# Kernel optimization log

Measured on AMD Instinct MI355X. Metric: run time of the kernel, lower is better.

Reference implementation:

```python
import jax, jax.numpy as jnp
import numpy as np

B, N, D, H = 256, 128, 2048, 16
DH = D // H  # 128 == N, required by the module's broadcast coefs*out


def setup_inputs() -> dict:
    key = jax.random.key(0)
    k0, k1, k2, k3, k4, k5 = jax.random.split(key, 6)
    batchinput = jax.random.normal(k0, (B, N, D), dtype=jnp.float32)
    # Conv1d(D, DH, 1, bias=False) == pointwise linear D -> DH
    Wa = jax.random.normal(k1, (D, DH), dtype=jnp.float32) * 0.02
    # Conv1d(DH, 1, 1) with bias
    Wb = jax.random.normal(k2, (DH, 1), dtype=jnp.float32) * 0.02
    bb = jax.random.normal(k3, (1,), dtype=jnp.float32) * 0.02
    Wc = jax.random.normal(k4, (DH, 1), dtype=jnp.float32) * 0.02
    bc = jax.random.normal(k5, (1,), dtype=jnp.float32) * 0.02
    bias = jnp.full((DH,), 0.01, dtype=jnp.float32)
    return {"batchinput": batchinput, "Wa": Wa, "Wb": Wb, "bb": bb,
            "Wc": Wc, "bc": bc, "bias": bias}


def reference(batchinput, Wa, Wb, bb, Wc, bc, bias):
    # All n_head heads share weights and dropout=0 -> identical; mean over heads
    # equals a single head. n_steps=1 (multi-step is shape-incompatible for H>1).
    h = jnp.einsum("bnd,de->bne", batchinput, Wa)          # [B,N,DH]
    t1 = h @ Wb + bb                                        # [B,N,1]
    t2 = h @ Wc + bc                                        # [B,N,1]
    # torch: temp1.permute -> [B,N,1]; temp2 stays [B,1,N]; broadcast add
    scores = t1 + jnp.swapaxes(t2, 1, 2)                    # [B,N,N]
    # F.softmax with dim=None on a 3D tensor -> dim=1
    coefs = jax.nn.softmax(jax.nn.leaky_relu(scores, negative_slope=0.2), axis=1)
    re = coefs * h + bias                                   # [B,N,N]*[B,N,DH], DH==N
    re = re + h                                             # residual=True
    return re
```

## Files before the change

### kernel.cpp

```cpp
#include <hip/hip_runtime.h>
#include <hip/hip_bf16.h>
#include <stdint.h>

typedef short bf16x8 __attribute__((ext_vector_type(8)));
typedef float f32x4  __attribute__((ext_vector_type(4)));

__device__ __forceinline__ unsigned short f2bf(float f) {
  unsigned int u = __float_as_uint(f);
  u = (u + 0x7fffu + ((u >> 16) & 1u)) >> 16;
  return (unsigned short)u;
}
__device__ __forceinline__ float bf2f(unsigned short s) { return __uint_as_float(((unsigned int)s) << 16); }
__device__ __forceinline__ float bflo(unsigned int pr) { return __uint_as_float(pr << 16); }
__device__ __forceinline__ float bfhi(unsigned int pr) { return __uint_as_float(pr & 0xffff0000u); }

#define Nn 128
#define Dd 2048
#define DH 128
#define BK 64
#define HP 130

__global__ void detect_dtype(const unsigned int* __restrict__ X, int* __restrict__ flag) {
  if (threadIdx.x == 0) {
    int cnt = 0;
#pragma unroll
    for (int i = 0; i < 64; ++i) {
      unsigned int e = (X[i] >> 23) & 0xffu;
      cnt += (e < 200u) ? 1 : 0;
    }
    *flag = (cnt >= 32) ? 1 : 0;
  }
}

__global__ __launch_bounds__(256) void transpose_wa(const void* __restrict__ Wa,
                                                    short* __restrict__ WaT,
                                                    const int* __restrict__ flag) {
  const int f32 = *flag;
  __shared__ short tile[32][33];
  const int tx = threadIdx.x & 31, ty = threadIdx.x >> 5;
  const int d0 = blockIdx.x * 32, e0 = blockIdx.y * 32;
#pragma unroll
  for (int r = 0; r < 4; ++r) {
    const int src = (d0 + ty + 8 * r) * DH + e0 + tx;
    short v;
    if (f32) v = (short)f2bf(((const float*)Wa)[src]);
    else     v = ((const short*)Wa)[src];
    tile[ty + 8 * r][tx] = v;
  }
  __syncthreads();
#pragma unroll
  for (int r = 0; r < 4; ++r)
    WaT[(e0 + ty + 8 * r) * Dd + d0 + tx] = tile[tx][ty + 8 * r];
}

union SMemU {
  struct { short A[128 * BK]; short Bm[128 * BK]; } st;
  unsigned short h[128 * HP];
};

template <bool F32>
__device__ __forceinline__ void gat_body(
    const void* __restrict__ Xv, const short* __restrict__ WaT,
    const void* __restrict__ Wb, const void* __restrict__ bbp,
    const void* __restrict__ Wc, const void* __restrict__ bcp,
    const void* __restrict__ biasp, void* __restrict__ outv,
    SMemU& sm, float* t1s, float* t2s, float* wbs, float* wcs,
    float* biass, float* red, float* mrec, float* srec)
{
  const int tid = threadIdx.x;
  const int b   = blockIdx.x;
  const int l   = tid & 63;
  const int w   = tid >> 6;
  const int wr  = w >> 1, wcol = w & 1;

  if (tid < 128) {
    wbs[tid]   = F32 ? ((const float*)Wb)[tid]    : bf2f(((const unsigned short*)Wb)[tid]);
    wcs[tid]   = F32 ? ((const float*)Wc)[tid]    : bf2f(((const unsigned short*)Wc)[tid]);
    biass[tid] = F32 ? ((const float*)biasp)[tid] : bf2f(((const unsigned short*)biasp)[tid]);
  }

  f32x4 acc[4][4];
#pragma unroll
  for (int i = 0; i < 4; ++i)
#pragma unroll
    for (int j = 0; j < 4; ++j) acc[i][j] = (f32x4){0.f, 0.f, 0.f, 0.f};

  const int rowi = tid >> 3;
  const int kofs = (tid & 7) * 8;
  short* As = sm.st.A;
  short* Bs = sm.st.Bm;
  const size_t xbase = (size_t)b * Nn * Dd;

  bf16x8 aV[4], bV[4];
  auto load_tiles = [&](int k0) {
#pragma unroll
    for (int c = 0; c < 4; ++c) {
      const int grow = (32 * c + rowi) * Dd + k0 + kofs;
      if (F32) {
        const float* p = (const float*)Xv + xbase + grow;
        float4 u0 = *(const float4*)p;
        float4 u1 = *(const float4*)(p + 4);
        bf16x8 t;
        t[0] = (short)f2bf(u0.x); t[1] = (short)f2bf(u0.y);
        t[2] = (short)f2bf(u0.z); t[3] = (short)f2bf(u0.w);
        t[4] = (short)f2bf(u1.x); t[5] = (short)f2bf(u1.y);
        t[6] = (short)f2bf(u1.z); t[7] = (short)f2bf(u1.w);
        aV[c] = t;
      } else {
        aV[c] = *(const bf16x8*)((const short*)Xv + xbase + grow);
      }
      bV[c] = *(const bf16x8*)(WaT + grow);
    }
  };

  load_tiles(0);
  for (int k0 = 0; k0 < Dd; k0 += BK) {
    __syncthreads();
#pragma unroll
    for (int c = 0; c < 4; ++c) {
      *(bf16x8*)&As[c * 2048 + tid * 8] = aV[c];
      *(bf16x8*)&Bs[c * 2048 + tid * 8] = bV[c];
    }
    __syncthreads();
    if (k0 + BK < Dd) load_tiles(k0 + BK);
#pragma unroll
    for (int ks = 0; ks < 2; ++ks) {
      bf16x8 aF[4], bF[4];
#pragma unroll
      for (int mr = 0; mr < 4; ++mr)
        aF[mr] = *(const bf16x8*)&As[(wr * 64 + mr * 16 + (l & 15)) * BK + ks * 32 + (l >> 4) * 8];
#pragma unroll
      for (int nc = 0; nc < 4; ++nc)
        bF[nc] = *(const bf16x8*)&Bs[(wcol * 64 + nc * 16 + (l & 15)) * BK + ks * 32 + (l >> 4) * 8];
#pragma unroll
      for (int mr = 0; mr < 4; ++mr)
#pragma unroll
        for (int nc = 0; nc < 4; ++nc)
          acc[mr][nc] = __builtin_amdgcn_mfma_f32_16x16x32_bf16(aF[mr], bF[nc], acc[mr][nc], 0, 0, 0);
    }
  }
  __syncthreads();

#pragma unroll
  for (int mr = 0; mr < 4; ++mr) {
    const int row0 = wr * 64 + mr * 16 + (l >> 4) * 4;
#pragma unroll
    for (int nc = 0; nc < 4; ++nc) {
      const int col = wcol * 64 + nc * 16 + (l & 15);
#pragma unroll
      for (int r = 0; r < 4; ++r)
        sm.h[(row0 + r) * HP + col] = f2bf(acc[mr][nc][r]);
    }
  }
  __syncthreads();

  {
    const int i = tid & 127;
    const float* wv = (tid < 128) ? wbs : wcs;
    const unsigned int* hr = (const unsigned int*)&sm.h[i * HP];
    float a0 = 0.f, a1 = 0.f;
#pragma unroll 4
    for (int e2 = 0; e2 < 64; ++e2) {
      const unsigned int pr = hr[e2];
      a0 += bflo(pr) * wv[2 * e2];
      a1 += bfhi(pr) * wv[2 * e2 + 1];
    }
    const void* bsel = (tid < 128) ? bbp : bcp;
    const float bbv = F32 ? ((const float*)bsel)[0] : bf2f(((const unsigned short*)bsel)[0]);
    const float t = a0 + a1 + bbv;
    if (tid < 128) t1s[i] = t; else t2s[i] = t;
  }
  __syncthreads();

  {
    const int j  = tid & 127;
    const int hf = tid >> 7;
    const float t2j = t2s[j];
    float mloc = -1e30f;
#pragma unroll 4
    for (int ii = 0; ii < 64; ++ii) {
      float s = t1s[hf * 64 + ii] + t2j;
      s = (s > 0.f) ? s : 0.2f * s;
      mloc = fmaxf(mloc, s);
    }
    red[hf * 128 + j] = mloc;
    __syncthreads();
    const float mj = fmaxf(red[j], red[128 + j]);
    float sl = 0.f;
#pragma unroll 4
    for (int ii = 0; ii < 64; ++ii) {
      float s = t1s[hf * 64 + ii] + t2j;
      s = (s > 0.f) ? s : 0.2f * s;
      sl += __expf(s - mj);
    }
    __syncthreads();
    red[hf * 128 + j] = sl;
    __syncthreads();
    if (hf == 0) {
      mrec[j] = mj;
      srec[j] = 1.f / (red[j] + red[128 + j]);
    }
  }
  __syncthreads();

  {
    const int jp = (tid & 63) * 2;
    const int rq = tid >> 6;
    const float m0 = mrec[jp],     s0 = srec[jp];
    const float m1 = mrec[jp + 1], s1 = srec[jp + 1];
    const float u0 = t2s[jp], u1 = t2s[jp + 1];
    const float b0 = biass[jp], b1 = biass[jp + 1];
#pragma unroll 4
    for (int ii = 0; ii < 32; ++ii) {
      const int i = ii * 4 + rq;
      const float t1i = t1s[i];
      float sA = t1i + u0; sA = (sA > 0.f) ? sA : 0.2f * sA;
      float sB = t1i + u1; sB = (sB > 0.f) ? sB : 0.2f * sB;
      const float pA = __expf(sA - m0) * s0;
      const float pB = __expf(sB - m1) * s1;
      const unsigned int pr = *(const unsigned int*)&sm.h[i * HP + jp];
      const float oA = bflo(pr) * (1.f + pA) + b0;
      const float oB = bfhi(pr) * (1.f + pB) + b1;
      if (F32) {
        float2 v2; v2.x = oA; v2.y = oB;
        *(float2*)((float*)outv + (size_t)b * Nn * DH + i * DH + jp) = v2;
      } else {
        const unsigned int pk = (unsigned int)f2bf(oA) | ((unsigned int)f2bf(oB) << 16);
        *(unsigned int*)((unsigned short*)outv + (size_t)b * Nn * DH + i * DH + jp) = pk;
      }
    }
  }
}

__global__ __launch_bounds__(256, 1) void fused_gat(
    const void* __restrict__ X, const short* __restrict__ WaT,
    const void* __restrict__ Wb, const void* __restrict__ bb,
    const void* __restrict__ Wc, const void* __restrict__ bc,
    const void* __restrict__ bias, void* __restrict__ out,
    const int* __restrict__ flag)
{
  __shared__ SMemU sm;
  __shared__ float t1s[128], t2s[128], wbs[128], wcs[128], biass[128];
  __shared__ float red[256], mrec[128], srec[128];
  if (*flag)
    gat_body<true>(X, WaT, Wb, bb, Wc, bc, bias, out, sm, t1s, t2s, wbs, wcs, biass, red, mrec, srec);
  else
    gat_body<false>(X, WaT, Wb, bb, Wc, bc, bias, out, sm, t1s, t2s, wbs, wcs, biass, red, mrec, srec);
}

extern "C" void kernel_launch(void* const* d_in, const int* in_sizes, int n_in,
                              void* d_out, int out_size, void* d_ws, size_t ws_size,
                              hipStream_t stream) {
  const void* X    = d_in[0];
  const void* Wa   = d_in[1];
  const void* Wb   = d_in[2];
  const void* bb   = d_in[3];
  const void* Wc   = d_in[4];
  const void* bc   = d_in[5];
  const void* bias = d_in[6];
  short* WaT = (short*)d_ws;
  int*   flag = (int*)((char*)d_ws + (512 << 10));

  detect_dtype<<<1, 64, 0, stream>>>((const unsigned int*)X, flag);
  transpose_wa<<<dim3(64, 4), 256, 0, stream>>>(Wa, WaT, flag);
  fused_gat<<<256, 256, 0, stream>>>(X, WaT, Wb, bb, Wc, bc, bias, d_out, flag);
}
```

Before: 409.1 us.

## Double-buffer LDS GEMM with swizzle, 512 threads, and fold dtype detection into kernels

The GEMM main loop now uses double-buffered LDS tiles with an XOR swizzle, so it needs one barrier per K-step instead of two. Global loads for the next tile are held in registers while MFMAs run on the current buffer. The block grows to 512 threads (8 waves, each owning a 64x32 output tile), and the epilogue phases are split across more threads. The separate detect kernel is removed: each kernel recomputes the dtype flag, and two specialized kernels are launched with the non-matching one exiting early. This adds a second full-grid launch that does nothing but early-exit, and LDS use for the tiles doubles.

```diff
diff --git a/kernel.cpp b/kernel.cpp
--- a/kernel.cpp
+++ b/kernel.cpp
@@ -4,15 +4,6 @@
 
 typedef short bf16x8 __attribute__((ext_vector_type(8)));
 typedef float f32x4  __attribute__((ext_vector_type(4)));
-
-__device__ __forceinline__ unsigned short f2bf(float f) {
-  unsigned int u = __float_as_uint(f);
-  u = (u + 0x7fffu + ((u >> 16) & 1u)) >> 16;
-  return (unsigned short)u;
-}
-__device__ __forceinline__ float bf2f(unsigned short s) { return __uint_as_float(((unsigned int)s) << 16); }
-__device__ __forceinline__ float bflo(unsigned int pr) { return __uint_as_float(pr << 16); }
-__device__ __forceinline__ float bfhi(unsigned int pr) { return __uint_as_float(pr & 0xffff0000u); }
 
 #define Nn 128
 #define Dd 2048
@@ -20,23 +11,33 @@
 #define BK 64
 #define HP 130
 
-__global__ void detect_dtype(const unsigned int* __restrict__ X, int* __restrict__ flag) {
-  if (threadIdx.x == 0) {
-    int cnt = 0;
-#pragma unroll
-    for (int i = 0; i < 64; ++i) {
-      unsigned int e = (X[i] >> 23) & 0xffu;
-      cnt += (e < 200u) ? 1 : 0;
-    }
-    *flag = (cnt >= 32) ? 1 : 0;
-  }
+__device__ __forceinline__ unsigned short f2bf(float f) {
+  unsigned int u = __float_as_uint(f);
+  u = (u + 0x7fffu + ((u >> 16) & 1u)) >> 16;
+  return (unsigned short)u;
+}
+__device__ __forceinline__ float bf2f(unsigned short s) { return __uint_as_float(((unsigned int)s) << 16); }
+__device__ __forceinline__ float bflo(unsigned int p) { return __uint_as_float(p << 16); }
+__device__ __forceinline__ float bfhi(unsigned int p) { return __uint_as_float(p & 0xffff0000u); }
+
+__device__ __forceinline__ int detect_f32(const unsigned int* __restrict__ X) {
+  int cnt = 0;
+#pragma unroll
+  for (int i = 0; i < 64; ++i) {
+    unsigned int e = (X[i] >> 23) & 0xffu;
+    cnt += (e < 200u) ? 1 : 0;
+  }
+  return cnt >= 32;
 }
 
 __global__ __launch_bounds__(256) void transpose_wa(const void* __restrict__ Wa,
                                                     short* __restrict__ WaT,
-                                                    const int* __restrict__ flag) {
-  const int f32 = *flag;
+                                                    const unsigned int* __restrict__ X) {
+  __shared__ int flg;
   __shared__ short tile[32][33];
+  if (threadIdx.x == 0) flg = detect_f32(X);
+  __syncthreads();
+  const int f32 = flg;
   const int tx = threadIdx.x & 31, ty = threadIdx.x >> 5;
   const int d0 = blockIdx.x * 32, e0 = blockIdx.y * 32;
 #pragma unroll
@@ -54,7 +55,7 @@
 }
 
 union SMemU {
-  struct { short A[128 * BK]; short Bm[128 * BK]; } st;
+  struct { short A[2][128 * BK]; short Bm[2][128 * BK]; } st;
   unsigned short h[128 * HP];
 };
 
@@ -63,15 +64,24 @@
     const void* __restrict__ Xv, const short* __restrict__ WaT,
     const void* __restrict__ Wb, const void* __restrict__ bbp,
     const void* __restrict__ Wc, const void* __restrict__ bcp,
-    const void* __restrict__ biasp, void* __restrict__ outv,
-    SMemU& sm, float* t1s, float* t2s, float* wbs, float* wcs,
-    float* biass, float* red, float* mrec, float* srec)
+    const void* __restrict__ biasp, void* __restrict__ outv)
 {
+  __shared__ SMemU sm;
+  __shared__ float t1s[128], t2s[128], wbs[128], wcs[128], biass[128];
+  __shared__ float red[512];
+  __shared__ float mrec[128], srec[128];
+  __shared__ int flg;
+
   const int tid = threadIdx.x;
+  if (tid == 0) flg = detect_f32((const unsigned int*)Xv);
+  __syncthreads();
+  if ((flg != 0) != F32) return;
+
   const int b   = blockIdx.x;
   const int l   = tid & 63;
   const int w   = tid >> 6;
-  const int wr  = w >> 1, wcol = w & 1;
+  const int wr  = w >> 2;
+  const int wc4 = w & 3;
 
   if (tid < 128) {
     wbs[tid]   = F32 ? ((const float*)Wb)[tid]    : bf2f(((const unsigned short*)Wb)[tid]);
@@ -79,74 +89,99 @@
     biass[tid] = F32 ? ((const float*)biasp)[tid] : bf2f(((const unsigned short*)biasp)[tid]);
   }
 
-  f32x4 acc[4][4];
+  f32x4 acc[4][2];
 #pragma unroll
   for (int i = 0; i < 4; ++i)
 #pragma unroll
-    for (int j = 0; j < 4; ++j) acc[i][j] = (f32x4){0.f, 0.f, 0.f, 0.f};
-
-  const int rowi = tid >> 3;
-  const int kofs = (tid & 7) * 8;
-  short* As = sm.st.A;
-  short* Bs = sm.st.Bm;
+    for (int j = 0; j < 2; ++j) acc[i][j] = (f32x4){0.f, 0.f, 0.f, 0.f};
+
+  const int rowh = tid >> 3;
+  const int g    = tid & 7;
   const size_t xbase = (size_t)b * Nn * Dd;
 
-  bf16x8 aV[4], bV[4];
-  auto load_tiles = [&](int k0) {
-#pragma unroll
-    for (int c = 0; c < 4; ++c) {
-      const int grow = (32 * c + rowi) * Dd + k0 + kofs;
+  float4 pa4[2][2];
+  bf16x8 paB[2];
+  bf16x8 pb[2];
+
+  auto load_g = [&](int k0) {
+#pragma unroll
+    for (int c = 0; c < 2; ++c) {
+      const int row = c * 64 + rowh;
+      const int off = row * Dd + k0 + g * 8;
       if (F32) {
-        const float* p = (const float*)Xv + xbase + grow;
-        float4 u0 = *(const float4*)p;
-        float4 u1 = *(const float4*)(p + 4);
-        bf16x8 t;
-        t[0] = (short)f2bf(u0.x); t[1] = (short)f2bf(u0.y);
-        t[2] = (short)f2bf(u0.z); t[3] = (short)f2bf(u0.w);
-        t[4] = (short)f2bf(u1.x); t[5] = (short)f2bf(u1.y);
-        t[6] = (short)f2bf(u1.z); t[7] = (short)f2bf(u1.w);
-        aV[c] = t;
+        const float* p = (const float*)Xv + xbase + off;
+        pa4[c][0] = *(const float4*)p;
+        pa4[c][1] = *(const float4*)(p + 4);
       } else {
-        aV[c] = *(const bf16x8*)((const short*)Xv + xbase + grow);
-      }
-      bV[c] = *(const bf16x8*)(WaT + grow);
+        paB[c] = *(const bf16x8*)((const short*)Xv + xbase + off);
+      }
+      pb[c] = *(const bf16x8*)(WaT + off);
     }
   };
 
-  load_tiles(0);
+  auto store_lds = [&](int p) {
+#pragma unroll
+    for (int c = 0; c < 2; ++c) {
+      const int row  = c * 64 + rowh;
+      const int phys = row * 64 + ((g ^ (row & 7)) << 3);
+      bf16x8 av;
+      if (F32) {
+        av[0] = (short)f2bf(pa4[c][0].x); av[1] = (short)f2bf(pa4[c][0].y);
+        av[2] = (short)f2bf(pa4[c][0].z); av[3] = (short)f2bf(pa4[c][0].w);
+        av[4] = (short)f2bf(pa4[c][1].x); av[5] = (short)f2bf(pa4[c][1].y);
+        av[6] = (short)f2bf(pa4[c][1].z); av[7] = (short)f2bf(pa4[c][1].w);
+      } else {
+        av = paB[c];
+      }
+      *(bf16x8*)&sm.st.A[p][phys]  = av;
+      *(bf16x8*)&sm.st.Bm[p][phys] = pb[c];
+    }
+  };
+
+  auto mfma_step = [&](int p) {
+#pragma unroll
+    for (int ks = 0; ks < 2; ++ks) {
+      const int gb = ks * 4 + (l >> 4);
+      bf16x8 aF[4], bF[2];
+#pragma unroll
+      for (int mr = 0; mr < 4; ++mr) {
+        const int row = wr * 64 + mr * 16 + (l & 15);
+        aF[mr] = *(const bf16x8*)&sm.st.A[p][row * 64 + ((gb ^ (row & 7)) << 3)];
+      }
+#pragma unroll
+      for (int nc = 0; nc < 2; ++nc) {
+        const int row = wc4 * 32 + nc * 16 + (l & 15);
+        bF[nc] = *(const bf16x8*)&sm.st.Bm[p][row * 64 + ((gb ^ (row & 7)) << 3)];
+      }
+#pragma unroll
+      for (int mr = 0; mr < 4; ++mr)
+#pragma unroll
+        for (int nc = 0; nc < 2; ++nc)
+          acc[mr][nc] = __builtin_amdgcn_mfma_f32_16x16x32_bf16(aF[mr], bF[nc], acc[mr][nc], 0, 0, 0);
+    }
+  };
+
+  load_g(0);
+  store_lds(0);
+  load_g(BK);
+  __syncthreads();
+  int p = 0;
   for (int k0 = 0; k0 < Dd; k0 += BK) {
+    mfma_step(p);
+    if (k0 + BK < Dd) {
+      store_lds(p ^ 1);
+      if (k0 + 2 * BK < Dd) load_g(k0 + 2 * BK);
+    }
     __syncthreads();
-#pragma unroll
-    for (int c = 0; c < 4; ++c) {
-      *(bf16x8*)&As[c * 2048 + tid * 8] = aV[c];
-      *(bf16x8*)&Bs[c * 2048 + tid * 8] = bV[c];
-    }
-    __syncthreads();
-    if (k0 + BK < Dd) load_tiles(k0 + BK);
-#pragma unroll
-    for (int ks = 0; ks < 2; ++ks) {
-      bf16x8 aF[4], bF[4];
-#pragma unroll
-      for (int mr = 0; mr < 4; ++mr)
-        aF[mr] = *(const bf16x8*)&As[(wr * 64 + mr * 16 + (l & 15)) * BK + ks * 32 + (l >> 4) * 8];
-#pragma unroll
-      for (int nc = 0; nc < 4; ++nc)
-        bF[nc] = *(const bf16x8*)&Bs[(wcol * 64 + nc * 16 + (l & 15)) * BK + ks * 32 + (l >> 4) * 8];
-#pragma unroll
-      for (int mr = 0; mr < 4; ++mr)
-#pragma unroll
-        for (int nc = 0; nc < 4; ++nc)
-          acc[mr][nc] = __builtin_amdgcn_mfma_f32_16x16x32_bf16(aF[mr], bF[nc], acc[mr][nc], 0, 0, 0);
-    }
-  }
-  __syncthreads();
+    p ^= 1;
+  }
 
 #pragma unroll
   for (int mr = 0; mr < 4; ++mr) {
     const int row0 = wr * 64 + mr * 16 + (l >> 4) * 4;
 #pragma unroll
-    for (int nc = 0; nc < 4; ++nc) {
-      const int col = wcol * 64 + nc * 16 + (l & 15);
+    for (int nc = 0; nc < 2; ++nc) {
+      const int col = wc4 * 32 + nc * 16 + (l & 15);
 #pragma unroll
       for (int r = 0; r < 4; ++r)
         sm.h[(row0 + r) * HP + col] = f2bf(acc[mr][nc][r]);
@@ -155,20 +190,27 @@
   __syncthreads();
 
   {
-    const int i = tid & 127;
-    const float* wv = (tid < 128) ? wbs : wcs;
-    const unsigned int* hr = (const unsigned int*)&sm.h[i * HP];
+    const int i    = (tid >> 1) & 127;
+    const int half = tid & 1;
+    const float* wv = ((tid < 256) ? wbs : wcs) + half * 64;
+    const unsigned int* hr = (const unsigned int*)&sm.h[i * HP] + half * 32;
     float a0 = 0.f, a1 = 0.f;
-#pragma unroll 4
-    for (int e2 = 0; e2 < 64; ++e2) {
+#pragma unroll 8
+    for (int e2 = 0; e2 < 32; ++e2) {
       const unsigned int pr = hr[e2];
       a0 += bflo(pr) * wv[2 * e2];
       a1 += bfhi(pr) * wv[2 * e2 + 1];
     }
-    const void* bsel = (tid < 128) ? bbp : bcp;
-    const float bbv = F32 ? ((const float*)bsel)[0] : bf2f(((const unsigned short*)bsel)[0]);
-    const float t = a0 + a1 + bbv;
-    if (tid < 128) t1s[i] = t; else t2s[i] = t;
+    red[tid] = a0 + a1;
+  }
+  __syncthreads();
+  if (tid < 256) {
+    const int j = tid & 127;
+    const int sel = tid >> 7;
+    const void* bsel = sel ? bcp : bbp;
+    const float bv = F32 ? ((const float*)bsel)[0] : bf2f(((const unsigned short*)bsel)[0]);
+    const float t = red[sel * 256 + 2 * j] + red[sel * 256 + 2 * j + 1] + bv;
+    if (sel == 0) t1s[j] = t; else t2s[j] = t;
   }
   __syncthreads();
 
@@ -177,19 +219,19 @@
     const int hf = tid >> 7;
     const float t2j = t2s[j];
     float mloc = -1e30f;
-#pragma unroll 4
-    for (int ii = 0; ii < 64; ++ii) {
-      float s = t1s[hf * 64 + ii] + t2j;
+#pragma unroll 8
+    for (int ii = 0; ii < 32; ++ii) {
+      float s = t1s[hf * 32 + ii] + t2j;
       s = (s > 0.f) ? s : 0.2f * s;
       mloc = fmaxf(mloc, s);
     }
     red[hf * 128 + j] = mloc;
     __syncthreads();
-    const float mj = fmaxf(red[j], red[128 + j]);
+    const float mj = fmaxf(fmaxf(red[j], red[128 + j]), fmaxf(red[256 + j], red[384 + j]));
     float sl = 0.f;
-#pragma unroll 4
-    for (int ii = 0; ii < 64; ++ii) {
-      float s = t1s[hf * 64 + ii] + t2j;
+#pragma unroll 8
+    for (int ii = 0; ii < 32; ++ii) {
+      float s = t1s[hf * 32 + ii] + t2j;
       s = (s > 0.f) ? s : 0.2f * s;
       sl += __expf(s - mj);
     }
@@ -198,7 +240,7 @@
     __syncthreads();
     if (hf == 0) {
       mrec[j] = mj;
-      srec[j] = 1.f / (red[j] + red[128 + j]);
+      srec[j] = 1.f / (red[j] + red[128 + j] + red[256 + j] + red[384 + j]);
     }
   }
   __syncthreads();
@@ -211,8 +253,8 @@
     const float u0 = t2s[jp], u1 = t2s[jp + 1];
     const float b0 = biass[jp], b1 = biass[jp + 1];
 #pragma unroll 4
-    for (int ii = 0; ii < 32; ++ii) {
-      const int i = ii * 4 + rq;
+    for (int ii = 0; ii < 16; ++ii) {
+      const int i = ii * 8 + rq;
       const float t1i = t1s[i];
       float sA = t1i + u0; sA = (sA > 0.f) ? sA : 0.2f * sA;
       float sB = t1i + u1; sB = (sB > 0.f) ? sB : 0.2f * sB;
@@ -232,20 +274,20 @@
   }
 }
 
-__global__ __launch_bounds__(256, 1) void fused_gat(
+__global__ __launch_bounds__(512, 2) void fused_gat_f32(
     const void* __restrict__ X, const short* __restrict__ WaT,
     const void* __restrict__ Wb, const void* __restrict__ bb,
     const void* __restrict__ Wc, const void* __restrict__ bc,
-    const void* __restrict__ bias, void* __restrict__ out,
-    const int* __restrict__ flag)
-{
-  __shared__ SMemU sm;
-  __shared__ float t1s[128], t2s[128], wbs[128], wcs[128], biass[128];
-  __shared__ float red[256], mrec[128], srec[128];
-  if (*flag)
-    gat_body<true>(X, WaT, Wb, bb, Wc, bc, bias, out, sm, t1s, t2s, wbs, wcs, biass, red, mrec, srec);
-  else
-    gat_body<false>(X, WaT, Wb, bb, Wc, bc, bias, out, sm, t1s, t2s, wbs, wcs, biass, red, mrec, srec);
+    const void* __restrict__ bias, void* __restrict__ out) {
+  gat_body<true>(X, WaT, Wb, bb, Wc, bc, bias, out);
+}
+
+__global__ __launch_bounds__(512, 2) void fused_gat_bf16(
+    const void* __restrict__ X, const short* __restrict__ WaT,
+    const void* __restrict__ Wb, const void* __restrict__ bb,
+    const void* __restrict__ Wc, const void* __restrict__ bc,
+    const void* __restrict__ bias, void* __restrict__ out) {
+  gat_body<false>(X, WaT, Wb, bb, Wc, bc, bias, out);
 }
 
 extern "C" void kernel_launch(void* const* d_in, const int* in_sizes, int n_in,
@@ -259,9 +301,8 @@
   const void* bc   = d_in[5];
   const void* bias = d_in[6];
   short* WaT = (short*)d_ws;
-  int*   flag = (int*)((char*)d_ws + (512 << 10));
-
-  detect_dtype<<<1, 64, 0, stream>>>((const unsigned int*)X, flag);
-  transpose_wa<<<dim3(64, 4), 256, 0, stream>>>(Wa, WaT, flag);
-  fused_gat<<<256, 256, 0, stream>>>(X, WaT, Wb, bb, Wc, bc, bias, d_out, flag);
-}
+
+  transpose_wa<<<dim3(64, 4), 256, 0, stream>>>(Wa, WaT, (const unsigned int*)X);
+  fused_gat_f32 <<<256, 512, 0, stream>>>(X, WaT, Wb, bb, Wc, bc, bias, d_out);
+  fused_gat_bf16<<<256, 512, 0, stream>>>(X, WaT, Wb, bb, Wc, bc, bias, d_out);
+}
```

Measured after the change: 403.8 us. No clear change (-1.3%).
